# Kernel optimization log

Measured on AMD Instinct MI355X. Metric: run time of the kernel, lower is better.

Reference implementation:

```python
import jax, jax.numpy as jnp
import numpy as np

WINDOW = 512
HOP = WINDOW // 2
N_COEFFS = WINDOW // 2 + 1
B, C, T = 4, 32, 131072


def setup_inputs() -> dict:
    key = jax.random.key(0)
    k1, k2, k3 = jax.random.split(key, 3)
    x = jax.random.normal(k1, (B, C, T), dtype=jnp.float32)
    # transfer parameter: magnitudes < 1 so the per-frame recurrence is stable
    transfer = jax.random.uniform(k2, (C, N_COEFFS), dtype=jnp.float32) * 0.9
    # mixer_matrix initialized as identity in the module; add small noise
    mixer_matrix = jnp.eye(C, dtype=jnp.float32) + 0.01 * jax.random.normal(k3, (C, C), dtype=jnp.float32)
    gain = jnp.ones((C,), dtype=jnp.float32)  # filled with gain=1.0
    return {"x": x, "transfer": transfer, "mixer_matrix": mixer_matrix, "gain": gain}


def reference(x, transfer, mixer_matrix, gain):
    Bb, Cc, Tt = x.shape
    # (x.permute(0,2,1) @ mixer).permute(0,2,1)
    x = jnp.einsum('bct,cd->bdt', x, mixer_matrix)

    # windowed_audio: frames of length WINDOW with hop HOP (pad tail with HOP zeros)
    xp = jnp.pad(x, ((0, 0), (0, 0), (0, HOP)))
    n_frames = Tt // HOP  # 512
    idx = jnp.arange(n_frames)[:, None] * HOP + jnp.arange(WINDOW)[None, :]  # [F, W]
    frames = xp[:, :, idx]  # [B, C, F, W]

    spec = jnp.fft.rfft(frames, axis=-1)  # [B, C, F, K] complex

    # sequential per-frame recurrence: out_i = (spec_i + out_{i-1}) * transfer
    spec_t = jnp.transpose(spec, (2, 0, 1, 3))  # [F, B, C, K]
    tr = transfer.astype(spec.dtype)[None, :, :]  # [1, C, K]

    def step(prev, s):
        cur = (s + prev) * tr
        return cur, cur

    _, outs = jax.lax.scan(step, jnp.zeros_like(spec_t[0]), spec_t)  # [F, B, C, K]
    out_spec = jnp.transpose(outs, (1, 2, 0, 3))  # [B, C, F, K]

    wins = jnp.fft.irfft(out_spec, n=WINDOW, axis=-1)  # [B, C, F, W]

    # overlap_add with (periodic) Hann window applied
    hann = (0.5 - 0.5 * jnp.cos(2.0 * jnp.pi * jnp.arange(WINDOW) / WINDOW)).astype(wins.dtype)
    wins = wins * hann
    out_len = n_frames * HOP + HOP
    flat_idx = idx.reshape(-1)
    samples = jnp.zeros((Bb, Cc, out_len), wins.dtype).at[:, :, flat_idx].add(
        wins.reshape(Bb, Cc, -1))

    samples = jnp.tanh(samples * gain[None, :, None])
    return samples[..., :Tt]
```

## Files before the change

kernel.cpp:

```cpp
#include <hip/hip_runtime.h>
#include <hip/hip_fp16.h>
#include <math.h>

#define T_LEN 131072
#define NCH   32
#define NBAT  4
#define WIN   512
#define HOP   256
#define NFR   512
#define NBIN  257
#define NBC   (NBAT*NCH)
#define FPB   4
#define NBLK  (NFR/FPB)
#define TWOPI 6.28318530717958647692f

#define SWZ(m) ((m) ^ ((((m) >> 4) & 15)))

__device__ __forceinline__ float2 cmul(float2 u, float2 v) {
  return make_float2(fmaf(u.x, v.x, -u.y * v.y), fmaf(u.x, v.y, u.y * v.x));
}

__device__ __forceinline__ float fast_tanh(float x) {
  float e = __expf(2.0f * x);
  return 1.0f - 2.0f * __builtin_amdgcn_rcpf(e + 1.0f);
}

__device__ __forceinline__ float2 h2f(__half2 h) { return __half22float2(h); }
__device__ __forceinline__ __half2 f2h(float2 f) { return __float22half2_rn(f); }

__device__ __forceinline__ void wave_sync() {
  asm volatile("" ::: "memory");
  __builtin_amdgcn_wave_barrier();
  asm volatile("" ::: "memory");
}

__device__ __forceinline__ void r4bf(float2 a, float2 b, float2 c, float2 d,
                                     float2& y0, float2& t1, float2& t2, float2& t3) {
  float2 apc = make_float2(a.x + c.x, a.y + c.y);
  float2 amc = make_float2(a.x - c.x, a.y - c.y);
  float2 bpd = make_float2(b.x + d.x, b.y + d.y);
  float2 bmd = make_float2(b.x - d.x, b.y - d.y);
  y0 = make_float2(apc.x + bpd.x, apc.y + bpd.y);
  t1 = make_float2(amc.x + bmd.y, amc.y - bmd.x);
  t2 = make_float2(apc.x - bpd.x, apc.y - bpd.y);
  t3 = make_float2(amc.x - bmd.y, amc.y + bmd.x);
}

struct TW {
  float2 a1, a2, a3, b1, b2, b3, c1, c2, c3;
};

__device__ __forceinline__ void load_tw(const float2* __restrict__ W256f, int lane, TW& t) {
  t.a1 = W256f[lane];     t.a2 = W256f[2 * lane];  t.a3 = W256f[3 * lane];
  int p1 = 4 * (lane >> 2);
  t.b1 = W256f[p1];       t.b2 = W256f[2 * p1];    t.b3 = W256f[3 * p1];
  int p2 = 16 * (lane >> 4);
  t.c1 = W256f[p2];       t.c2 = W256f[2 * p2];    t.c3 = W256f[3 * p2];
}

__device__ __forceinline__ void fft256_reg(float2& z0, float2& z1, float2& z2, float2& z3,
                                           float2* __restrict__ buf, int lane, const TW& tw) {
  float2 y0, t1, t2, t3;
  r4bf(z0, z1, z2, z3, y0, t1, t2, t3);
  int o0 = 4 * lane;
  buf[SWZ(o0)]     = y0;
  buf[SWZ(o0 + 1)] = cmul(tw.a1, t1);
  buf[SWZ(o0 + 2)] = cmul(tw.a2, t2);
  buf[SWZ(o0 + 3)] = cmul(tw.a3, t3);
  wave_sync();
  {
    float2 a = buf[SWZ(lane)], b = buf[SWZ(lane + 64)],
           c = buf[SWZ(lane + 128)], d = buf[SWZ(lane + 192)];
    wave_sync();
    r4bf(a, b, c, d, y0, t1, t2, t3);
    int o = lane + 12 * (lane >> 2);
    buf[SWZ(o)]      = y0;
    buf[SWZ(o + 4)]  = cmul(tw.b1, t1);
    buf[SWZ(o + 8)]  = cmul(tw.b2, t2);
    buf[SWZ(o + 12)] = cmul(tw.b3, t3);
  }
  wave_sync();
  {
    float2 a = buf[SWZ(lane)], b = buf[SWZ(lane + 64)],
           c = buf[SWZ(lane + 128)], d = buf[SWZ(lane + 192)];
    wave_sync();
    r4bf(a, b, c, d, y0, t1, t2, t3);
    int o = lane + 48 * (lane >> 4);
    buf[SWZ(o)]      = y0;
    buf[SWZ(o + 16)] = cmul(tw.c1, t1);
    buf[SWZ(o + 32)] = cmul(tw.c2, t2);
    buf[SWZ(o + 48)] = cmul(tw.c3, t3);
  }
  wave_sync();
  {
    float2 a = buf[SWZ(lane)], b = buf[SWZ(lane + 64)],
           c = buf[SWZ(lane + 128)], d = buf[SWZ(lane + 192)];
    wave_sync();
    r4bf(a, b, c, d, z0, z1, z2, z3);
  }
}

__device__ __forceinline__ void build_tables(float2* W256f, float2* W512s) {
  int tid = threadIdx.x;
  float sv, cv;
  __sincosf(-(TWOPI / 256.0f) * (float)tid, &sv, &cv);
  W256f[tid] = make_float2(cv, sv);
  __sincosf(-(TWOPI / 512.0f) * (float)tid, &sv, &cv);
  W512s[tid] = make_float2(cv, sv);
  if (tid == 0) W512s[256] = make_float2(-1.f, 0.f);
}

__global__ __launch_bounds__(256) void mix_kernel(const float* __restrict__ x,
                                                  const float* __restrict__ mixer,
                                                  __half2* __restrict__ y) {
  __shared__ float mm[NCH][NCH];
  for (int i = threadIdx.x; i < NCH * NCH; i += 256)
    ((float*)mm)[i] = mixer[i];
  __syncthreads();
  int b = blockIdx.y;
  int t2 = blockIdx.x * 256 + threadIdx.x;
  const float2* xv = (const float2*)x;
  float2 xr[NCH];
#pragma unroll
  for (int c = 0; c < NCH; c++)
    xr[c] = xv[(((size_t)(b * NCH + c)) * T_LEN >> 1) + t2];
#pragma unroll 4
  for (int d = 0; d < NCH; d++) {
    float ax = 0.f, ay = 0.f;
#pragma unroll
    for (int c = 0; c < NCH; c++) {
      ax = fmaf(xr[c].x, mm[c][d], ax);
      ay = fmaf(xr[c].y, mm[c][d], ay);
    }
    y[(((size_t)(b * NCH + d)) * T_LEN >> 1) + t2] = f2h(make_float2(ax, ay));
  }
}

__global__ __launch_bounds__(256) void fft_fwd_kernel(const __half2* __restrict__ y,
                                                      const float* __restrict__ transfer,
                                                      __half2* __restrict__ spec) {
  __shared__ float2 fbuf[FPB][NBIN];
  __shared__ float2 W256f[256];
  __shared__ float2 W512s[NBIN];
  build_tables(W256f, W512s);
  __syncthreads();
  int wave = threadIdx.x >> 6, lane = threadIdx.x & 63;
  int cid = blockIdx.x * FPB + wave;
  int bc = cid >> 7, blk = cid & (NBLK - 1);
  int ch = bc & (NCH - 1);
  float2* buf = fbuf[wave];
  TW tw; load_tw(W256f, lane, tw);
  float cwq[4], swq[4], trq[4];
#pragma unroll
  for (int q = 0; q < 4; q++) {
    int k = lane + 64 * q;
    cwq[q] = W512s[k].x; swq[q] = W512s[k].y;
    trq[q] = transfer[ch * NBIN + k];
  }
  float tr256 = transfer[ch * NBIN + 256];
  float2 s[4] = {make_float2(0,0), make_float2(0,0), make_float2(0,0), make_float2(0,0)};
  float s256x = 0.f;
  size_t base2 = ((size_t)bc * T_LEN + (size_t)blk * (FPB * HOP)) >> 1;
  size_t fb = ((size_t)bc * NFR + (size_t)blk * FPB) * NBIN;
  bool lastchunk = (blk == NBLK - 1);
#pragma unroll
  for (int j = 0; j < FPB; j++) {
    const __half2* src = y + base2 + (size_t)j * (HOP / 2);
    float2 z0 = h2f(src[lane]);
    float2 z1 = h2f(src[lane + 64]);
    float2 z2, z3;
    if (lastchunk && j == FPB - 1) {
      z2 = make_float2(0, 0); z3 = make_float2(0, 0);
    } else {
      z2 = h2f(src[lane + 128]);
      z3 = h2f(src[lane + 192]);
    }
    fft256_reg(z0, z1, z2, z3, buf, lane, tw);
    buf[lane] = z0; buf[lane + 64] = z1; buf[lane + 128] = z2; buf[lane + 192] = z3;
    wave_sync();
    float2 zm0 = buf[(256 - lane) & 255];
    float2 zm1 = buf[192 - lane];
    float2 zm2 = buf[128 - lane];
    float2 zm3 = buf[64 - lane];
    float2 z0b = buf[0];
    wave_sync();
#pragma unroll
    for (int q = 0; q < 4; q++) {
      float2 zk  = (q == 0) ? z0 : (q == 1) ? z1 : (q == 2) ? z2 : z3;
      float2 zmk = (q == 0) ? zm0 : (q == 1) ? zm1 : (q == 2) ? zm2 : zm3;
      float Ex = 0.5f * (zk.x + zmk.x), Ey = 0.5f * (zk.y - zmk.y);
      float dx = 0.5f * (zk.x - zmk.x), dy = 0.5f * (zk.y + zmk.y);
      float Ox = dy, Oy = -dx;
      float Yx = Ex + Ox * cwq[q] - Oy * swq[q];
      float Yy = Ey + Ox * swq[q] + Oy * cwq[q];
      s[q].x = trq[q] * (Yx + s[q].x);
      s[q].y = trq[q] * (Yy + s[q].y);
      spec[fb + (size_t)j * NBIN + lane + 64 * q] = f2h(s[q]);
    }
    s256x = tr256 * ((z0b.x - z0b.y) + s256x);
    if (lane == 0) spec[fb + (size_t)j * NBIN + 256] = f2h(make_float2(s256x, 0.f));
    wave_sync();
  }
}

__global__ __launch_bounds__(256) void carry_kernel(const __half2* __restrict__ spec,
                                                    const float* __restrict__ transfer,
                                                    __half2* __restrict__ carries) {
  int tid = blockIdx.x * 256 + threadIdx.x;
  if (tid >= NBC * NBIN) return;
  int bc = tid / NBIN, k = tid - bc * NBIN;
  int ch = bc & (NCH - 1);
  float tr = transfer[ch * NBIN + k];
  float tr2 = tr * tr;
  float tr4 = tr2 * tr2;
  const __half2* fin = spec + (size_t)bc * NFR * NBIN + (size_t)(FPB - 1) * NBIN + k;
  __half2* cp = carries + (size_t)bc * NBLK * NBIN + k;
  float cx = 0.f, cy = 0.f;
  for (int i = 0; i < NBLK; i += 8) {
    float2 v[8];
#pragma unroll
    for (int u = 0; u < 8; u++) v[u] = h2f(fin[(size_t)(i + u) * FPB * NBIN]);
#pragma unroll
    for (int u = 0; u < 8; u++) {
      cp[(size_t)(i + u) * NBIN] = f2h(make_float2(cx, cy));
      cx = v[u].x + tr4 * cx;
      cy = v[u].y + tr4 * cy;
    }
  }
}

__global__ __launch_bounds__(256) void fft_inv_kernel(const __half2* __restrict__ spec,
                                                      const __half2* __restrict__ carries,
                                                      const float* __restrict__ transfer,
                                                      const float* __restrict__ gain,
                                                      float* __restrict__ out,
                                                      __half2* __restrict__ bnd) {
  __shared__ float2 fbuf[FPB][NBIN];
  __shared__ float2 W256f[256];
  __shared__ float2 W512s[NBIN];
  build_tables(W256f, W512s);
  __syncthreads();
  int wave = threadIdx.x >> 6, lane = threadIdx.x & 63;
  int cid = blockIdx.x * FPB + wave;
  int bc = cid >> 7, blk = cid & (NBLK - 1);
  int ch = bc & (NCH - 1);
  float2* buf = fbuf[wave];
  TW tw; load_tw(W256f, lane, tw);
  const __half2* crp = carries + ((size_t)bc * NBLK + blk) * NBIN;
  float cwq[4], swq[4], trq[4], trp[4], h0[4], h1[4];
  float2 cv[4];
#pragma unroll
  for (int q = 0; q < 4; q++) {
    int k = lane + 64 * q;
    cwq[q] = W512s[k].x; swq[q] = -W512s[k].y;
    trq[q] = transfer[ch * NBIN + k];
    trp[q] = trq[q];
    cv[q] = h2f(crp[k]);
    int t0 = 2 * k, t1 = 2 * k + 1;
    int i0 = (t0 <= 256) ? t0 : 512 - t0;
    int i1 = (t1 <= 256) ? t1 : 512 - t1;
    h0[q] = (0.5f - 0.5f * W512s[i0].x) * (1.0f / 256.0f);
    h1[q] = (0.5f - 0.5f * W512s[i1].x) * (1.0f / 256.0f);
  }
  float tr256 = transfer[ch * NBIN + 256], trp256 = tr256;
  float2 cv256 = h2f(crp[256]);
  float g = gain[ch];
  const __half2* sp0 = spec + ((size_t)bc * NFR + (size_t)blk * FPB) * NBIN;
  float2* outv = (float2*)out;
  size_t obase2 = ((size_t)bc * T_LEN + (size_t)blk * (FPB * HOP)) >> 1;
  __half2* bp = bnd + (((size_t)bc * NBLK + blk) * 2) * (HOP / 2);
  float2 pt0, pt1;
#pragma unroll
  for (int j = 0; j < FPB; j++) {
    const __half2* sp = sp0 + (size_t)j * NBIN;
    float2 Y0 = h2f(sp[lane]);       Y0.x = fmaf(trp[0], cv[0].x, Y0.x); Y0.y = fmaf(trp[0], cv[0].y, Y0.y);
    float2 Y1 = h2f(sp[lane + 64]);  Y1.x = fmaf(trp[1], cv[1].x, Y1.x); Y1.y = fmaf(trp[1], cv[1].y, Y1.y);
    float2 Y2 = h2f(sp[lane + 128]); Y2.x = fmaf(trp[2], cv[2].x, Y2.x); Y2.y = fmaf(trp[2], cv[2].y, Y2.y);
    float2 Y3 = h2f(sp[lane + 192]); Y3.x = fmaf(trp[3], cv[3].x, Y3.x); Y3.y = fmaf(trp[3], cv[3].y, Y3.y);
    float2 y256 = h2f(sp[256]);
    y256.x = fmaf(trp256, cv256.x, y256.x);
    y256.y = fmaf(trp256, cv256.y, y256.y);
#pragma unroll
    for (int q = 0; q < 4; q++) trp[q] *= trq[q];
    trp256 *= tr256;
    buf[lane] = Y0; buf[lane + 64] = Y1; buf[lane + 128] = Y2; buf[lane + 192] = Y3;
    if (lane == 0) buf[256] = y256;
    wave_sync();
    float2 ym0 = buf[256 - lane];
    float2 ym1 = buf[192 - lane];
    float2 ym2 = buf[128 - lane];
    float2 ym3 = buf[64 - lane];
    wave_sync();
    float2 z0, z1, z2, z3;
#pragma unroll
    for (int q = 0; q < 4; q++) {
      float2 yk  = (q == 0) ? Y0 : (q == 1) ? Y1 : (q == 2) ? Y2 : Y3;
      float2 ymk = (q == 0) ? ym0 : (q == 1) ? ym1 : (q == 2) ? ym2 : ym3;
      float Ex = 0.5f * (yk.x + ymk.x), Ey = 0.5f * (yk.y - ymk.y);
      float dx = 0.5f * (yk.x - ymk.x), dy = 0.5f * (yk.y + ymk.y);
      float Ox = dx * cwq[q] - dy * swq[q];
      float Oy = dx * swq[q] + dy * cwq[q];
      float2 zq = make_float2(Ex - Oy, -(Ey + Ox));
      if (q == 0) z0 = zq; else if (q == 1) z1 = zq; else if (q == 2) z2 = zq; else z3 = zq;
    }
    fft256_reg(z0, z1, z2, z3, buf, lane, tw);
    float2 w0 = make_float2(z0.x * h0[0], -z0.y * h1[0]);
    float2 w1 = make_float2(z1.x * h0[1], -z1.y * h1[1]);
    float2 w2 = make_float2(z2.x * h0[2], -z2.y * h1[2]);
    float2 w3 = make_float2(z3.x * h0[3], -z3.y * h1[3]);
    if (j == 0) {
      bp[lane]      = f2h(w0);
      bp[lane + 64] = f2h(w1);
    } else {
      float2 v0 = make_float2(pt0.x + w0.x, pt0.y + w0.y);
      float2 v1 = make_float2(pt1.x + w1.x, pt1.y + w1.y);
      outv[obase2 + (size_t)j * 128 + lane] =
          make_float2(fast_tanh(g * v0.x), fast_tanh(g * v0.y));
      outv[obase2 + (size_t)j * 128 + lane + 64] =
          make_float2(fast_tanh(g * v1.x), fast_tanh(g * v1.y));
    }
    pt0 = w2; pt1 = w3;
    wave_sync();
  }
  bp[128 + lane] = f2h(pt0);
  bp[192 + lane] = f2h(pt1);
}

__global__ __launch_bounds__(256) void final_kernel(const __half* __restrict__ bnd,
                                                    const float* __restrict__ gain,
                                                    float* __restrict__ out) {
  int bc = blockIdx.y, b = blockIdx.x;
  int s = threadIdx.x;
  const __half* base = bnd + ((size_t)bc * NBLK) * 2 * HOP;
  float v = __half2float(base[((size_t)b * 2) * HOP + s]);
  if (b > 0) v += __half2float(base[((size_t)(b - 1) * 2 + 1) * HOP + s]);
  float g = gain[bc & (NCH - 1)];
  out[(size_t)bc * T_LEN + (size_t)b * (FPB * HOP) + s] = fast_tanh(g * v);
}

extern "C" void kernel_launch(void* const* d_in, const int* in_sizes, int n_in,
                              void* d_out, int out_size, void* d_ws, size_t ws_size,
                              hipStream_t stream) {
  (void)in_sizes; (void)n_in; (void)out_size; (void)ws_size;
  const float* x        = (const float*)d_in[0];
  const float* transfer = (const float*)d_in[1];
  const float* mixer    = (const float*)d_in[2];
  const float* gain     = (const float*)d_in[3];
  float* out = (float*)d_out;

  char* p = (char*)d_ws;
  __half2* spec    = (__half2*)p;                       p += (size_t)NBC * NFR * NBIN * 4;
  __half2* bnd     = (__half2*)p;                       p += (size_t)NBC * NBLK * 2 * HOP * 2;
  __half2* carries = (__half2*)p;                       p += (size_t)NBC * NBLK * NBIN * 4;
  __half2* y       = (__half2*)p;

  mix_kernel<<<dim3(T_LEN / 512, NBAT), 256, 0, stream>>>(x, mixer, y);
  fft_fwd_kernel<<<dim3(NBC * NBLK / FPB), 256, 0, stream>>>(y, transfer, spec);
  carry_kernel<<<dim3((NBC * NBIN + 255) / 256), 256, 0, stream>>>(spec, transfer, carries);
  fft_inv_kernel<<<dim3(NBC * NBLK / FPB), 256, 0, stream>>>(spec, carries, transfer, gain, out, (__half2*)bnd);
  final_kernel<<<dim3(NBLK, NBC), 256, 0, stream>>>((const __half*)bnd, gain, out);
}
```

Before: 121.3 us.

## Double frames per wave chunk, prefetch next frame, and drop FFT half-scaling

Each wave now processes 8 consecutive frames instead of 4, which halves the number of chunk carries and shortens the serial carry scan. The carry kernel is updated to a tr^8 stride with 16-wide batches. Both FFT kernels now prefetch the next frame's inputs into registers while the current frame is transformed, and they carry a launch-bounds occupancy hint. The 0.5 factors in the real-FFT split are removed and compensated elsewhere (the Nyquist term is doubled, the Hann scale goes from 1/256 to 1/1024). The cost is more serial work per wave, fewer total waves, and higher register pressure.

```diff
diff --git a/kernel.cpp b/kernel.cpp
--- a/kernel.cpp
+++ b/kernel.cpp
@@ -10,7 +10,7 @@
 #define NFR   512
 #define NBIN  257
 #define NBC   (NBAT*NCH)
-#define FPB   4
+#define FPB   8
 #define NBLK  (NFR/FPB)
 #define TWOPI 6.28318530717958647692f
 
@@ -136,17 +136,17 @@
   }
 }
 
-__global__ __launch_bounds__(256) void fft_fwd_kernel(const __half2* __restrict__ y,
-                                                      const float* __restrict__ transfer,
-                                                      __half2* __restrict__ spec) {
-  __shared__ float2 fbuf[FPB][NBIN];
+__global__ __launch_bounds__(256, 4) void fft_fwd_kernel(const __half2* __restrict__ y,
+                                                         const float* __restrict__ transfer,
+                                                         __half2* __restrict__ spec) {
+  __shared__ float2 fbuf[4][NBIN];
   __shared__ float2 W256f[256];
   __shared__ float2 W512s[NBIN];
   build_tables(W256f, W512s);
   __syncthreads();
   int wave = threadIdx.x >> 6, lane = threadIdx.x & 63;
-  int cid = blockIdx.x * FPB + wave;
-  int bc = cid >> 7, blk = cid & (NBLK - 1);
+  int cid = blockIdx.x * 4 + wave;
+  int bc = cid >> 6, blk = cid & (NBLK - 1);
   int ch = bc & (NCH - 1);
   float2* buf = fbuf[wave];
   TW tw; load_tw(W256f, lane, tw);
@@ -163,18 +163,27 @@
   size_t base2 = ((size_t)bc * T_LEN + (size_t)blk * (FPB * HOP)) >> 1;
   size_t fb = ((size_t)bc * NFR + (size_t)blk * FPB) * NBIN;
   bool lastchunk = (blk == NBLK - 1);
-#pragma unroll
-  for (int j = 0; j < FPB; j++) {
-    const __half2* src = y + base2 + (size_t)j * (HOP / 2);
-    float2 z0 = h2f(src[lane]);
-    float2 z1 = h2f(src[lane + 64]);
-    float2 z2, z3;
-    if (lastchunk && j == FPB - 1) {
-      z2 = make_float2(0, 0); z3 = make_float2(0, 0);
-    } else {
-      z2 = h2f(src[lane + 128]);
-      z3 = h2f(src[lane + 192]);
-    }
+  const __half2* src = y + base2;
+  float2 c0 = h2f(src[lane]);
+  float2 c1 = h2f(src[lane + 64]);
+  float2 c2 = h2f(src[lane + 128]);
+  float2 c3 = h2f(src[lane + 192]);
+#pragma unroll 2
+  for (int j = 0; j < FPB; ++j) {
+    float2 n0, n1, n2, n3;
+    bool have_next = (j + 1 < FPB);
+    if (have_next) {
+      const __half2* s2 = src + (size_t)(j + 1) * (HOP / 2);
+      n0 = h2f(s2[lane]);
+      n1 = h2f(s2[lane + 64]);
+      if (lastchunk && (j + 1 == FPB - 1)) {
+        n2 = make_float2(0, 0); n3 = make_float2(0, 0);
+      } else {
+        n2 = h2f(s2[lane + 128]);
+        n3 = h2f(s2[lane + 192]);
+      }
+    }
+    float2 z0 = c0, z1 = c1, z2 = c2, z3 = c3;
     fft256_reg(z0, z1, z2, z3, buf, lane, tw);
     buf[lane] = z0; buf[lane + 64] = z1; buf[lane + 128] = z2; buf[lane + 192] = z3;
     wave_sync();
@@ -188,8 +197,8 @@
     for (int q = 0; q < 4; q++) {
       float2 zk  = (q == 0) ? z0 : (q == 1) ? z1 : (q == 2) ? z2 : z3;
       float2 zmk = (q == 0) ? zm0 : (q == 1) ? zm1 : (q == 2) ? zm2 : zm3;
-      float Ex = 0.5f * (zk.x + zmk.x), Ey = 0.5f * (zk.y - zmk.y);
-      float dx = 0.5f * (zk.x - zmk.x), dy = 0.5f * (zk.y + zmk.y);
+      float Ex = zk.x + zmk.x, Ey = zk.y - zmk.y;
+      float dx = zk.x - zmk.x, dy = zk.y + zmk.y;
       float Ox = dy, Oy = -dx;
       float Yx = Ex + Ox * cwq[q] - Oy * swq[q];
       float Yy = Ey + Ox * swq[q] + Oy * cwq[q];
@@ -197,9 +206,10 @@
       s[q].y = trq[q] * (Yy + s[q].y);
       spec[fb + (size_t)j * NBIN + lane + 64 * q] = f2h(s[q]);
     }
-    s256x = tr256 * ((z0b.x - z0b.y) + s256x);
+    s256x = tr256 * (2.0f * (z0b.x - z0b.y) + s256x);
     if (lane == 0) spec[fb + (size_t)j * NBIN + 256] = f2h(make_float2(s256x, 0.f));
     wave_sync();
+    if (have_next) { c0 = n0; c1 = n1; c2 = n2; c3 = n3; }
   }
 }
 
@@ -213,36 +223,37 @@
   float tr = transfer[ch * NBIN + k];
   float tr2 = tr * tr;
   float tr4 = tr2 * tr2;
+  float tr8 = tr4 * tr4;
   const __half2* fin = spec + (size_t)bc * NFR * NBIN + (size_t)(FPB - 1) * NBIN + k;
   __half2* cp = carries + (size_t)bc * NBLK * NBIN + k;
   float cx = 0.f, cy = 0.f;
-  for (int i = 0; i < NBLK; i += 8) {
-    float2 v[8];
-#pragma unroll
-    for (int u = 0; u < 8; u++) v[u] = h2f(fin[(size_t)(i + u) * FPB * NBIN]);
-#pragma unroll
-    for (int u = 0; u < 8; u++) {
+  for (int i = 0; i < NBLK; i += 16) {
+    float2 v[16];
+#pragma unroll
+    for (int u = 0; u < 16; u++) v[u] = h2f(fin[(size_t)(i + u) * FPB * NBIN]);
+#pragma unroll
+    for (int u = 0; u < 16; u++) {
       cp[(size_t)(i + u) * NBIN] = f2h(make_float2(cx, cy));
-      cx = v[u].x + tr4 * cx;
-      cy = v[u].y + tr4 * cy;
-    }
-  }
-}
-
-__global__ __launch_bounds__(256) void fft_inv_kernel(const __half2* __restrict__ spec,
-                                                      const __half2* __restrict__ carries,
-                                                      const float* __restrict__ transfer,
-                                                      const float* __restrict__ gain,
-                                                      float* __restrict__ out,
-                                                      __half2* __restrict__ bnd) {
-  __shared__ float2 fbuf[FPB][NBIN];
+      cx = v[u].x + tr8 * cx;
+      cy = v[u].y + tr8 * cy;
+    }
+  }
+}
+
+__global__ __launch_bounds__(256, 4) void fft_inv_kernel(const __half2* __restrict__ spec,
+                                                         const __half2* __restrict__ carries,
+                                                         const float* __restrict__ transfer,
+                                                         const float* __restrict__ gain,
+                                                         float* __restrict__ out,
+                                                         __half2* __restrict__ bnd) {
+  __shared__ float2 fbuf[4][NBIN];
   __shared__ float2 W256f[256];
   __shared__ float2 W512s[NBIN];
   build_tables(W256f, W512s);
   __syncthreads();
   int wave = threadIdx.x >> 6, lane = threadIdx.x & 63;
-  int cid = blockIdx.x * FPB + wave;
-  int bc = cid >> 7, blk = cid & (NBLK - 1);
+  int cid = blockIdx.x * 4 + wave;
+  int bc = cid >> 6, blk = cid & (NBLK - 1);
   int ch = bc & (NCH - 1);
   float2* buf = fbuf[wave];
   TW tw; load_tw(W256f, lane, tw);
@@ -259,8 +270,8 @@
     int t0 = 2 * k, t1 = 2 * k + 1;
     int i0 = (t0 <= 256) ? t0 : 512 - t0;
     int i1 = (t1 <= 256) ? t1 : 512 - t1;
-    h0[q] = (0.5f - 0.5f * W512s[i0].x) * (1.0f / 256.0f);
-    h1[q] = (0.5f - 0.5f * W512s[i1].x) * (1.0f / 256.0f);
+    h0[q] = (0.5f - 0.5f * W512s[i0].x) * (1.0f / 1024.0f);
+    h1[q] = (0.5f - 0.5f * W512s[i1].x) * (1.0f / 1024.0f);
   }
   float tr256 = transfer[ch * NBIN + 256], trp256 = tr256;
   float2 cv256 = h2f(crp[256]);
@@ -270,14 +281,28 @@
   size_t obase2 = ((size_t)bc * T_LEN + (size_t)blk * (FPB * HOP)) >> 1;
   __half2* bp = bnd + (((size_t)bc * NBLK + blk) * 2) * (HOP / 2);
   float2 pt0, pt1;
-#pragma unroll
-  for (int j = 0; j < FPB; j++) {
-    const __half2* sp = sp0 + (size_t)j * NBIN;
-    float2 Y0 = h2f(sp[lane]);       Y0.x = fmaf(trp[0], cv[0].x, Y0.x); Y0.y = fmaf(trp[0], cv[0].y, Y0.y);
-    float2 Y1 = h2f(sp[lane + 64]);  Y1.x = fmaf(trp[1], cv[1].x, Y1.x); Y1.y = fmaf(trp[1], cv[1].y, Y1.y);
-    float2 Y2 = h2f(sp[lane + 128]); Y2.x = fmaf(trp[2], cv[2].x, Y2.x); Y2.y = fmaf(trp[2], cv[2].y, Y2.y);
-    float2 Y3 = h2f(sp[lane + 192]); Y3.x = fmaf(trp[3], cv[3].x, Y3.x); Y3.y = fmaf(trp[3], cv[3].y, Y3.y);
-    float2 y256 = h2f(sp[256]);
+  float2 C0 = h2f(sp0[lane]);
+  float2 C1 = h2f(sp0[lane + 64]);
+  float2 C2 = h2f(sp0[lane + 128]);
+  float2 C3 = h2f(sp0[lane + 192]);
+  float2 C256 = h2f(sp0[256]);
+#pragma unroll 2
+  for (int j = 0; j < FPB; ++j) {
+    float2 N0, N1, N2, N3, N256;
+    bool have_next = (j + 1 < FPB);
+    if (have_next) {
+      const __half2* sp = sp0 + (size_t)(j + 1) * NBIN;
+      N0 = h2f(sp[lane]);
+      N1 = h2f(sp[lane + 64]);
+      N2 = h2f(sp[lane + 128]);
+      N3 = h2f(sp[lane + 192]);
+      N256 = h2f(sp[256]);
+    }
+    float2 Y0 = C0; Y0.x = fmaf(trp[0], cv[0].x, Y0.x); Y0.y = fmaf(trp[0], cv[0].y, Y0.y);
+    float2 Y1 = C1; Y1.x = fmaf(trp[1], cv[1].x, Y1.x); Y1.y = fmaf(trp[1], cv[1].y, Y1.y);
+    float2 Y2 = C2; Y2.x = fmaf(trp[2], cv[2].x, Y2.x); Y2.y = fmaf(trp[2], cv[2].y, Y2.y);
+    float2 Y3 = C3; Y3.x = fmaf(trp[3], cv[3].x, Y3.x); Y3.y = fmaf(trp[3], cv[3].y, Y3.y);
+    float2 y256 = C256;
     y256.x = fmaf(trp256, cv256.x, y256.x);
     y256.y = fmaf(trp256, cv256.y, y256.y);
 #pragma unroll
@@ -296,8 +321,8 @@
     for (int q = 0; q < 4; q++) {
       float2 yk  = (q == 0) ? Y0 : (q == 1) ? Y1 : (q == 2) ? Y2 : Y3;
       float2 ymk = (q == 0) ? ym0 : (q == 1) ? ym1 : (q == 2) ? ym2 : ym3;
-      float Ex = 0.5f * (yk.x + ymk.x), Ey = 0.5f * (yk.y - ymk.y);
-      float dx = 0.5f * (yk.x - ymk.x), dy = 0.5f * (yk.y + ymk.y);
+      float Ex = yk.x + ymk.x, Ey = yk.y - ymk.y;
+      float dx = yk.x - ymk.x, dy = yk.y + ymk.y;
       float Ox = dx * cwq[q] - dy * swq[q];
       float Oy = dx * swq[q] + dy * cwq[q];
       float2 zq = make_float2(Ex - Oy, -(Ey + Ox));
@@ -321,6 +346,7 @@
     }
     pt0 = w2; pt1 = w3;
     wave_sync();
+    if (have_next) { C0 = N0; C1 = N1; C2 = N2; C3 = N3; C256 = N256; }
   }
   bp[128 + lane] = f2h(pt0);
   bp[192 + lane] = f2h(pt1);
@@ -355,8 +381,8 @@
   __half2* y       = (__half2*)p;
 
   mix_kernel<<<dim3(T_LEN / 512, NBAT), 256, 0, stream>>>(x, mixer, y);
-  fft_fwd_kernel<<<dim3(NBC * NBLK / FPB), 256, 0, stream>>>(y, transfer, spec);
+  fft_fwd_kernel<<<dim3(NBC * NBLK / 4), 256, 0, stream>>>(y, transfer, spec);
   carry_kernel<<<dim3((NBC * NBIN + 255) / 256), 256, 0, stream>>>(spec, transfer, carries);
-  fft_inv_kernel<<<dim3(NBC * NBLK / FPB), 256, 0, stream>>>(spec, carries, transfer, gain, out, (__half2*)bnd);
+  fft_inv_kernel<<<dim3(NBC * NBLK / 4), 256, 0, stream>>>(spec, carries, transfer, gain, out, (__half2*)bnd);
   final_kernel<<<dim3(NBLK, NBC), 256, 0, stream>>>((const __half*)bnd, gain, out);
 }
```

New measurement: 171.6 us. +41.4%, slower.
